# Optimization experiments

Hardware: AMD Instinct MI355X
Metric: run time of the kernel (lower is better)

The kernel has to match this reference:

```python
import jax, jax.numpy as jnp
import numpy as np

EMBED_DIM = 8
THRESHOLD = 0.8
N_NODES = 8192
# QCNNModel (stack of FC layers mimicking quantum conv/pool steps):
# 8 -> 16 -> 16 -> 12 -> 8 -> 4 -> 1, tanh hidden activations, sigmoid head.
QCNN_DIMS = [8, 16, 16, 12, 8, 4, 1]


def setup_inputs() -> dict:
    key = jax.random.key(0)
    ks = jax.random.split(key, 20)
    inp = {
        "inputs": jax.random.normal(ks[0], (N_NODES, EMBED_DIM), dtype=jnp.float32),
        "rotation": jax.random.normal(ks[1], (EMBED_DIM, EMBED_DIM), dtype=jnp.float32),
        "entangle": jax.random.normal(ks[2], (EMBED_DIM, EMBED_DIM), dtype=jnp.float32),
        "gnn_w": jax.random.normal(ks[3], (EMBED_DIM, EMBED_DIM), dtype=jnp.float32) * 0.3,
        "gnn_b": jnp.zeros((EMBED_DIM,), dtype=jnp.float32),
    }
    for li in range(len(QCNN_DIMS) - 1):
        din, dout = QCNN_DIMS[li], QCNN_DIMS[li + 1]
        inp[f"qw{li}"] = jax.random.normal(ks[4 + 2 * li], (dout, din), dtype=jnp.float32) * (1.0 / np.sqrt(din))
        inp[f"qb{li}"] = jnp.zeros((dout,), dtype=jnp.float32)
    return inp


def _forward(inputs, rotation, entangle, gnn_w, gnn_b, qws, qbs):
    n = inputs.shape[0]
    # --- fidelity adjacency (vectorized Gram matrix + threshold) ---
    x = inputs / (jnp.linalg.norm(inputs, axis=1, keepdims=True) + 1e-12)
    fid = jnp.square(x @ x.T)                      # [n, n] |<i|j>|^2
    eye = jnp.eye(n, dtype=bool)
    adj = jnp.where((fid >= THRESHOLD) & ~eye, 1.0, 0.0).astype(inputs.dtype)
    # --- graph diffusion: neighbour sum + linear + relu ---
    neighbour_sum = adj @ inputs                   # [n, d]
    diffused = jax.nn.relu(neighbour_sum @ gnn_w.T + gnn_b)
    # --- self-attention (query=rotation, key=entangle, value=features) ---
    q = diffused @ rotation                        # [n, d]
    k = diffused @ entangle                        # [n, d]
    scores = jax.nn.softmax((q @ k.T) / jnp.sqrt(jnp.asarray(EMBED_DIM, inputs.dtype)), axis=-1)
    attended = scores @ diffused                   # [n, d]
    # --- QCNN fully-connected stack ---
    h = attended
    n_layers = len(qws)
    for li in range(n_layers):
        h = h @ qws[li].T + qbs[li]
        h = jax.nn.tanh(h) if li < n_layers - 1 else jax.nn.sigmoid(h)
    return h                                       # [n, 1]


def reference(inputs, rotation, entangle, gnn_w, gnn_b,
              qw0, qb0, qw1, qb1, qw2, qb2, qw3, qb3, qw4, qb4, qw5, qb5):
    qws = [qw0, qw1, qw2, qw3, qw4, qw5]
    qbs = [qb0, qb1, qb2, qb3, qb4, qb5]
    return _forward(inputs, rotation, entangle, gnn_w, gnn_b, qws, qbs)
```

## Files before the change

### kernel.cpp

```cpp
#include <hip/hip_runtime.h>
#include <math.h>

#define NN 8192

__device__ __forceinline__ float fexp2(float x) {
    float r;
    asm("v_exp_f32 %0, %1" : "=v"(r) : "v"(x));
    return r;
}

__global__ __launch_bounds__(256) void k_norm(const float* __restrict__ in,
                                              float* __restrict__ xn) {
    int r = blockIdx.x * 256 + threadIdx.x;
    const float4* p = reinterpret_cast<const float4*>(in + (size_t)r * 8);
    float4 a = p[0], b = p[1];
    float ss = a.x*a.x + a.y*a.y + a.z*a.z + a.w*a.w
             + b.x*b.x + b.y*b.y + b.z*b.z + b.w*b.w;
    float inv = 1.0f / (sqrtf(ss) + 1e-12f);
    a.x *= inv; a.y *= inv; a.z *= inv; a.w *= inv;
    b.x *= inv; b.y *= inv; b.z *= inv; b.w *= inv;
    float4* o = reinterpret_cast<float4*>(xn + (size_t)r * 8);
    o[0] = a; o[1] = b;
}

template<int SEGS>
__global__ __launch_bounds__(256) void k_adj_t(const float* __restrict__ xn,
                                               const float* __restrict__ in,
                                               float* __restrict__ pns) {
    constexpr int JC = NN / SEGS;
    constexpr int RSTR = NN / 2;
    __shared__ float4 sx[JC * 2];
    __shared__ float4 si[JC * 2];
    int tid = threadIdx.x;
    int r = blockIdx.x * 256 + tid;
    int seg = blockIdx.y;
    int j0 = seg * JC;

    for (int idx = tid; idx < JC * 2; idx += 256) {
        sx[idx] = reinterpret_cast<const float4*>(xn + (size_t)j0 * 8)[idx];
        si[idx] = reinterpret_cast<const float4*>(in + (size_t)j0 * 8)[idx];
    }
    float x[2][8];
    #pragma unroll
    for (int i = 0; i < 2; ++i) {
        const float4* xp = reinterpret_cast<const float4*>(xn + (size_t)(r + i * RSTR) * 8);
        float4 a = xp[0], b = xp[1];
        x[i][0]=a.x; x[i][1]=a.y; x[i][2]=a.z; x[i][3]=a.w;
        x[i][4]=b.x; x[i][5]=b.y; x[i][6]=b.z; x[i][7]=b.w;
    }
    __syncthreads();

    float A[2][8] = {};

    for (int c8 = 0; c8 < JC; c8 += 8) {
        #pragma unroll
        for (int u = 0; u < 8; ++u) {
            int t = c8 + u;
            int j = j0 + t;
            float4 a = sx[t * 2], b = sx[t * 2 + 1];
            bool hit[2];
            bool hany = false;
            #pragma unroll
            for (int i = 0; i < 2; ++i) {
                float d = fmaf(x[i][7], b.w, fmaf(x[i][6], b.z,
                          fmaf(x[i][5], b.y, fmaf(x[i][4], b.x,
                          fmaf(x[i][3], a.w, fmaf(x[i][2], a.z,
                          fmaf(x[i][1], a.y, x[i][0] * a.x)))))));
                hit[i] = (d * d >= 0.8f) && (j != r + i * RSTR);
                hany = hany || hit[i];
            }
            if (hany) {
                float4 u0 = si[t * 2], u1 = si[t * 2 + 1];
                #pragma unroll
                for (int i = 0; i < 2; ++i) {
                    if (hit[i]) {
                        A[i][0]+=u0.x; A[i][1]+=u0.y; A[i][2]+=u0.z; A[i][3]+=u0.w;
                        A[i][4]+=u1.x; A[i][5]+=u1.y; A[i][6]+=u1.z; A[i][7]+=u1.w;
                    }
                }
            }
        }
    }
    #pragma unroll
    for (int i = 0; i < 2; ++i) {
        float4* o = reinterpret_cast<float4*>(pns + ((size_t)(r + i * RSTR) * SEGS + seg) * 8);
        o[0] = make_float4(A[i][0], A[i][1], A[i][2], A[i][3]);
        o[1] = make_float4(A[i][4], A[i][5], A[i][6], A[i][7]);
    }
}

template<int NSEG>
__global__ __launch_bounds__(256) void k_diff3(const float* __restrict__ pns,
                                               const float* __restrict__ gw,
                                               const float* __restrict__ gb,
                                               const float* __restrict__ rot,
                                               const float* __restrict__ ent,
                                               float* __restrict__ dif,
                                               float* __restrict__ qsb,
                                               float* __restrict__ kkb) {
    int tid = threadIdx.x;
    int sub = tid & 31;
    int row = blockIdx.x * 8 + (tid >> 5);
    float ns[8] = {0,0,0,0,0,0,0,0};
    #pragma unroll
    for (int it = 0; it < NSEG / 32; ++it) {
        int g = sub + it * 32;
        const float4* p = reinterpret_cast<const float4*>(pns + ((size_t)row * NSEG + g) * 8);
        float4 a = p[0], b = p[1];
        ns[0]+=a.x; ns[1]+=a.y; ns[2]+=a.z; ns[3]+=a.w;
        ns[4]+=b.x; ns[5]+=b.y; ns[6]+=b.z; ns[7]+=b.w;
    }
    #pragma unroll
    for (int msk = 1; msk <= 16; msk <<= 1) {
        #pragma unroll
        for (int e = 0; e < 8; ++e) ns[e] += __shfl_xor(ns[e], msk);
    }
    if (sub == 0) {
        float df[8];
        #pragma unroll
        for (int d = 0; d < 8; ++d) {
            float v = gb[d];
            #pragma unroll
            for (int e = 0; e < 8; ++e) v += ns[e] * gw[d * 8 + e];
            df[d] = fmaxf(v, 0.0f);
        }
        const float QSC = (float)(1.4426950408889634 / 2.8284271247461903);
        #pragma unroll
        for (int d = 0; d < 8; ++d) {
            float vq = 0.0f, vk = 0.0f;
            #pragma unroll
            for (int e = 0; e < 8; ++e) {
                vq += df[e] * rot[e * 8 + d];
                vk += df[e] * ent[e * 8 + d];
            }
            qsb[(size_t)row * 8 + d] = vq * QSC;
            kkb[(size_t)row * 8 + d] = vk;
        }
        float4* o = reinterpret_cast<float4*>(dif + (size_t)row * 8);
        o[0] = make_float4(df[0], df[1], df[2], df[3]);
        o[1] = make_float4(df[4], df[5], df[6], df[7]);
    }
}

template<int SEGS>
__global__ __launch_bounds__(256) void k_attn_t(const float* __restrict__ qsb,
                                                const float* __restrict__ kkb,
                                                const float* __restrict__ dif,
                                                float* __restrict__ pacc,
                                                float* __restrict__ pm,
                                                float* __restrict__ psum) {
    constexpr int JC = NN / SEGS;
    constexpr int RSTR = NN / 2;
    __shared__ float4 sk[JC * 2];
    __shared__ float4 sd[JC * 2];
    int tid = threadIdx.x;
    int r = blockIdx.x * 256 + tid;
    int seg = blockIdx.y;
    int j0 = seg * JC;

    for (int idx = tid; idx < JC * 2; idx += 256) {
        sk[idx] = reinterpret_cast<const float4*>(kkb + (size_t)j0 * 8)[idx];
        sd[idx] = reinterpret_cast<const float4*>(dif + (size_t)j0 * 8)[idx];
    }
    float q[2][8];
    #pragma unroll
    for (int i = 0; i < 2; ++i) {
        const float4* qp = reinterpret_cast<const float4*>(qsb + (size_t)(r + i * RSTR) * 8);
        float4 a = qp[0], b = qp[1];
        q[i][0]=a.x; q[i][1]=a.y; q[i][2]=a.z; q[i][3]=a.w;
        q[i][4]=b.x; q[i][5]=b.y; q[i][6]=b.z; q[i][7]=b.w;
    }
    __syncthreads();

    float m[2], sum[2];
    float A[2][8] = {};
    #pragma unroll
    for (int i = 0; i < 2; ++i) { m[i] = -__builtin_huge_valf(); sum[i] = 0.0f; }

    for (int c8 = 0; c8 < JC; c8 += 8) {
        float s[2][8];
        #pragma unroll
        for (int u = 0; u < 8; ++u) {
            int t = c8 + u;
            float4 ka = sk[t * 2], kb = sk[t * 2 + 1];
            #pragma unroll
            for (int i = 0; i < 2; ++i) {
                s[i][u] = fmaf(q[i][7], kb.w, fmaf(q[i][6], kb.z,
                          fmaf(q[i][5], kb.y, fmaf(q[i][4], kb.x,
                          fmaf(q[i][3], ka.w, fmaf(q[i][2], ka.z,
                          fmaf(q[i][1], ka.y, q[i][0] * ka.x)))))));
            }
        }
        #pragma unroll
        for (int i = 0; i < 2; ++i) {
            float cm = fmaxf(fmaxf(fmaxf(s[i][0], s[i][1]), fmaxf(s[i][2], s[i][3])),
                             fmaxf(fmaxf(s[i][4], s[i][5]), fmaxf(s[i][6], s[i][7])));
            float mn = fmaxf(m[i], cm);
            float rs = fexp2(m[i] - mn);
            m[i] = mn;
            sum[i] *= rs;
            #pragma unroll
            for (int e = 0; e < 8; ++e) A[i][e] *= rs;
        }
        #pragma unroll
        for (int u = 0; u < 8; ++u) {
            int t = c8 + u;
            float4 da = sd[t * 2], db = sd[t * 2 + 1];
            #pragma unroll
            for (int i = 0; i < 2; ++i) {
                float p = fexp2(s[i][u] - m[i]);
                sum[i] += p;
                A[i][0] = fmaf(p, da.x, A[i][0]); A[i][1] = fmaf(p, da.y, A[i][1]);
                A[i][2] = fmaf(p, da.z, A[i][2]); A[i][3] = fmaf(p, da.w, A[i][3]);
                A[i][4] = fmaf(p, db.x, A[i][4]); A[i][5] = fmaf(p, db.y, A[i][5]);
                A[i][6] = fmaf(p, db.z, A[i][6]); A[i][7] = fmaf(p, db.w, A[i][7]);
            }
        }
    }

    #pragma unroll
    for (int i = 0; i < 2; ++i) {
        size_t b = (size_t)(r + i * RSTR) * SEGS + seg;
        float4* o = reinterpret_cast<float4*>(pacc + b * 8);
        o[0] = make_float4(A[i][0], A[i][1], A[i][2], A[i][3]);
        o[1] = make_float4(A[i][4], A[i][5], A[i][6], A[i][7]);
        pm[b] = m[i];
        psum[b] = sum[i];
    }
}

template<int NSEG>
__global__ __launch_bounds__(256) void k_merge3(const float* __restrict__ pacc,
                                                const float* __restrict__ pm,
                                                const float* __restrict__ psum,
                                                const float* __restrict__ qw0, const float* __restrict__ qb0,
                                                const float* __restrict__ qw1, const float* __restrict__ qb1,
                                                const float* __restrict__ qw2, const float* __restrict__ qb2,
                                                const float* __restrict__ qw3, const float* __restrict__ qb3,
                                                const float* __restrict__ qw4, const float* __restrict__ qb4,
                                                const float* __restrict__ qw5, const float* __restrict__ qb5,
                                                float* __restrict__ out) {
    int tid = threadIdx.x;
    int sub = tid & 31;
    int row = blockIdx.x * 8 + (tid >> 5);

    float m = -3.0e38f, T = 0.0f;
    float A[8] = {0,0,0,0,0,0,0,0};
    #pragma unroll
    for (int it = 0; it < NSEG / 32; ++it) {
        int g = sub + it * 32;
        size_t base = (size_t)row * NSEG + g;
        float mg = pm[base];
        float newm = fmaxf(m, mg);
        float cs = fexp2(m - newm);
        float cg = fexp2(mg - newm);
        T = fmaf(T, cs, psum[base] * cg);
        const float4* p = reinterpret_cast<const float4*>(pacc + base * 8);
        float4 a = p[0], b = p[1];
        A[0] = fmaf(A[0], cs, a.x * cg); A[1] = fmaf(A[1], cs, a.y * cg);
        A[2] = fmaf(A[2], cs, a.z * cg); A[3] = fmaf(A[3], cs, a.w * cg);
        A[4] = fmaf(A[4], cs, b.x * cg); A[5] = fmaf(A[5], cs, b.y * cg);
        A[6] = fmaf(A[6], cs, b.z * cg); A[7] = fmaf(A[7], cs, b.w * cg);
        m = newm;
    }
    #pragma unroll
    for (int msk = 1; msk <= 16; msk <<= 1) {
        float mo = __shfl_xor(m, msk);
        float To = __shfl_xor(T, msk);
        float Ao[8];
        #pragma unroll
        for (int e = 0; e < 8; ++e) Ao[e] = __shfl_xor(A[e], msk);
        float newm = fmaxf(m, mo);
        float cs = fexp2(m - newm);
        float co = fexp2(mo - newm);
        T = T * cs + To * co;
        #pragma unroll
        for (int e = 0; e < 8; ++e) A[e] = A[e] * cs + Ao[e] * co;
        m = newm;
    }

    if (sub == 0) {
        float invT = 1.0f / T;
        float h0[8];
        #pragma unroll
        for (int d = 0; d < 8; ++d) h0[d] = A[d] * invT;

        float h1[16];
        #pragma unroll
        for (int t = 0; t < 16; ++t) {
            float v = qb0[t];
            #pragma unroll
            for (int e = 0; e < 8; ++e) v += h0[e] * qw0[t * 8 + e];
            h1[t] = tanhf(v);
        }
        float h2[16];
        #pragma unroll
        for (int t = 0; t < 16; ++t) {
            float v = qb1[t];
            #pragma unroll
            for (int e = 0; e < 16; ++e) v += h1[e] * qw1[t * 16 + e];
            h2[t] = tanhf(v);
        }
        float h3[12];
        #pragma unroll
        for (int t = 0; t < 12; ++t) {
            float v = qb2[t];
            #pragma unroll
            for (int e = 0; e < 16; ++e) v += h2[e] * qw2[t * 16 + e];
            h3[t] = tanhf(v);
        }
        float h4[8];
        #pragma unroll
        for (int t = 0; t < 8; ++t) {
            float v = qb3[t];
            #pragma unroll
            for (int e = 0; e < 12; ++e) v += h3[e] * qw3[t * 12 + e];
            h4[t] = tanhf(v);
        }
        float h5[4];
        #pragma unroll
        for (int t = 0; t < 4; ++t) {
            float v = qb4[t];
            #pragma unroll
            for (int e = 0; e < 8; ++e) v += h4[e] * qw4[t * 8 + e];
            h5[t] = tanhf(v);
        }
        float o = qb5[0];
        #pragma unroll
        for (int e = 0; e < 4; ++e) o += h5[e] * qw5[e];
        out[row] = 1.0f / (1.0f + expf(-o));
    }
}

extern "C" void kernel_launch(void* const* d_in, const int* in_sizes, int n_in,
                              void* d_out, int out_size, void* d_ws, size_t ws_size,
                              hipStream_t stream) {
    const float* in  = (const float*)d_in[0];
    const float* rot = (const float*)d_in[1];
    const float* ent = (const float*)d_in[2];
    const float* gw  = (const float*)d_in[3];
    const float* gb  = (const float*)d_in[4];
    const float* qw0 = (const float*)d_in[5];
    const float* qb0 = (const float*)d_in[6];
    const float* qw1 = (const float*)d_in[7];
    const float* qb1 = (const float*)d_in[8];
    const float* qw2 = (const float*)d_in[9];
    const float* qb2 = (const float*)d_in[10];
    const float* qw3 = (const float*)d_in[11];
    const float* qb3 = (const float*)d_in[12];
    const float* qw4 = (const float*)d_in[13];
    const float* qb4 = (const float*)d_in[14];
    const float* qw5 = (const float*)d_in[15];
    const float* qb5 = (const float*)d_in[16];

    auto need = [](int nseg) { return ((size_t)NN * 8 * 4 + (size_t)nseg * NN * 18) * 4; };
    const int nseg = (ws_size >= need(64)) ? 64 : 32;

    float* ws = (float*)d_ws;
    size_t off = 0;
    float* xn   = ws + off; off += (size_t)NN * 8;
    float* pns  = ws + off; off += (size_t)nseg * NN * 8;
    float* dif  = ws + off; off += (size_t)NN * 8;
    float* qsb  = ws + off; off += (size_t)NN * 8;
    float* kkb  = ws + off; off += (size_t)NN * 8;
    float* pacc = ws + off; off += (size_t)nseg * NN * 8;
    float* pm   = ws + off; off += (size_t)nseg * NN;
    float* psum = ws + off; off += (size_t)nseg * NN;

    dim3 blk(256);
    k_norm<<<dim3(NN / 256), blk, 0, stream>>>(in, xn);
    if (nseg == 64) {
        k_adj_t<64><<<dim3(NN / 2 / 256, 64), blk, 0, stream>>>(xn, in, pns);
        k_diff3<64><<<dim3(NN / 8), blk, 0, stream>>>(pns, gw, gb, rot, ent, dif, qsb, kkb);
        k_attn_t<64><<<dim3(NN / 2 / 256, 64), blk, 0, stream>>>(qsb, kkb, dif, pacc, pm, psum);
        k_merge3<64><<<dim3(NN / 8), blk, 0, stream>>>(pacc, pm, psum,
                                                       qw0, qb0, qw1, qb1, qw2, qb2,
                                                       qw3, qb3, qw4, qb4, qw5, qb5,
                                                       (float*)d_out);
    } else {
        k_adj_t<32><<<dim3(NN / 2 / 256, 32), blk, 0, stream>>>(xn, in, pns);
        k_diff3<32><<<dim3(NN / 8), blk, 0, stream>>>(pns, gw, gb, rot, ent, dif, qsb, kkb);
        k_attn_t<32><<<dim3(NN / 2 / 256, 32), blk, 0, stream>>>(qsb, kkb, dif, pacc, pm, psum);
        k_merge3<32><<<dim3(NN / 8), blk, 0, stream>>>(pacc, pm, psum,
                                                       qw0, qb0, qw1, qb1, qw2, qb2,
                                                       qw3, qb3, qw4, qb4, qw5, qb5,
                                                       (float*)d_out);
    }
}
```

Baseline: 100.8 us.

## Run attention QK^T and PV on fp16 MFMA with padded transposed operands

Replaces the scalar fp32 flash-style attention kernel with one that computes scores and the probability-value product via 16x16x16 fp16 MFMA instructions, one wave per 16 query rows. The diffusion kernel now emits fp16 Q/K padded to 16 dims and a transposed fp16 value matrix in place of the fp32 buffers. The aim is to move the O(N^2) dot-product and accumulation work onto matrix cores and cut the LDS traffic. In exchange it reads K and V straight from global memory without LDS staging, doubles the padded work, and lowers the precision of scores and probabilities to fp16.

```diff
diff --git a/kernel.cpp b/kernel.cpp
--- a/kernel.cpp
+++ b/kernel.cpp
@@ -2,6 +2,9 @@
 #include <math.h>
 
 #define NN 8192
+
+typedef _Float16 h4v __attribute__((ext_vector_type(4)));
+typedef float f4v __attribute__((ext_vector_type(4)));
 
 __device__ __forceinline__ float fexp2(float x) {
     float r;
@@ -95,9 +98,9 @@
                                                const float* __restrict__ gb,
                                                const float* __restrict__ rot,
                                                const float* __restrict__ ent,
-                                               float* __restrict__ dif,
-                                               float* __restrict__ qsb,
-                                               float* __restrict__ kkb) {
+                                               _Float16* __restrict__ qhp,
+                                               _Float16* __restrict__ khp,
+                                               _Float16* __restrict__ difT) {
     int tid = threadIdx.x;
     int sub = tid & 31;
     int row = blockIdx.x * 8 + (tid >> 5);
@@ -133,99 +136,75 @@
                 vq += df[e] * rot[e * 8 + d];
                 vk += df[e] * ent[e * 8 + d];
             }
-            qsb[(size_t)row * 8 + d] = vq * QSC;
-            kkb[(size_t)row * 8 + d] = vk;
-        }
-        float4* o = reinterpret_cast<float4*>(dif + (size_t)row * 8);
-        o[0] = make_float4(df[0], df[1], df[2], df[3]);
-        o[1] = make_float4(df[4], df[5], df[6], df[7]);
+            qhp[(size_t)row * 16 + d] = (_Float16)(vq * QSC);
+            khp[(size_t)row * 16 + d] = (_Float16)vk;
+            difT[(size_t)d * NN + row] = (_Float16)df[d];
+        }
+        #pragma unroll
+        for (int d = 8; d < 16; ++d) {
+            qhp[(size_t)row * 16 + d] = (_Float16)0.0f;
+            khp[(size_t)row * 16 + d] = (_Float16)0.0f;
+            difT[(size_t)d * NN + row] = (_Float16)0.0f;
+        }
     }
 }
 
 template<int SEGS>
-__global__ __launch_bounds__(256) void k_attn_t(const float* __restrict__ qsb,
-                                                const float* __restrict__ kkb,
-                                                const float* __restrict__ dif,
+__global__ __launch_bounds__(256) void k_attn_m(const _Float16* __restrict__ qhp,
+                                                const _Float16* __restrict__ khp,
+                                                const _Float16* __restrict__ difT,
                                                 float* __restrict__ pacc,
                                                 float* __restrict__ pm,
                                                 float* __restrict__ psum) {
     constexpr int JC = NN / SEGS;
-    constexpr int RSTR = NN / 2;
-    __shared__ float4 sk[JC * 2];
-    __shared__ float4 sd[JC * 2];
     int tid = threadIdx.x;
-    int r = blockIdx.x * 256 + tid;
+    int lane = tid & 63;
+    int w = tid >> 6;
+    int qbase = (blockIdx.x * 4 + w) * 16;
     int seg = blockIdx.y;
     int j0 = seg * JC;
-
-    for (int idx = tid; idx < JC * 2; idx += 256) {
-        sk[idx] = reinterpret_cast<const float4*>(kkb + (size_t)j0 * 8)[idx];
-        sd[idx] = reinterpret_cast<const float4*>(dif + (size_t)j0 * 8)[idx];
-    }
-    float q[2][8];
-    #pragma unroll
-    for (int i = 0; i < 2; ++i) {
-        const float4* qp = reinterpret_cast<const float4*>(qsb + (size_t)(r + i * RSTR) * 8);
-        float4 a = qp[0], b = qp[1];
-        q[i][0]=a.x; q[i][1]=a.y; q[i][2]=a.z; q[i][3]=a.w;
-        q[i][4]=b.x; q[i][5]=b.y; q[i][6]=b.z; q[i][7]=b.w;
-    }
-    __syncthreads();
-
-    float m[2], sum[2];
-    float A[2][8] = {};
-    #pragma unroll
-    for (int i = 0; i < 2; ++i) { m[i] = -__builtin_huge_valf(); sum[i] = 0.0f; }
-
-    for (int c8 = 0; c8 < JC; c8 += 8) {
-        float s[2][8];
-        #pragma unroll
-        for (int u = 0; u < 8; ++u) {
-            int t = c8 + u;
-            float4 ka = sk[t * 2], kb = sk[t * 2 + 1];
-            #pragma unroll
-            for (int i = 0; i < 2; ++i) {
-                s[i][u] = fmaf(q[i][7], kb.w, fmaf(q[i][6], kb.z,
-                          fmaf(q[i][5], kb.y, fmaf(q[i][4], kb.x,
-                          fmaf(q[i][3], ka.w, fmaf(q[i][2], ka.z,
-                          fmaf(q[i][1], ka.y, q[i][0] * ka.x)))))));
-            }
-        }
-        #pragma unroll
-        for (int i = 0; i < 2; ++i) {
-            float cm = fmaxf(fmaxf(fmaxf(s[i][0], s[i][1]), fmaxf(s[i][2], s[i][3])),
-                             fmaxf(fmaxf(s[i][4], s[i][5]), fmaxf(s[i][6], s[i][7])));
-            float mn = fmaxf(m[i], cm);
-            float rs = fexp2(m[i] - mn);
-            m[i] = mn;
-            sum[i] *= rs;
-            #pragma unroll
-            for (int e = 0; e < 8; ++e) A[i][e] *= rs;
-        }
-        #pragma unroll
-        for (int u = 0; u < 8; ++u) {
-            int t = c8 + u;
-            float4 da = sd[t * 2], db = sd[t * 2 + 1];
-            #pragma unroll
-            for (int i = 0; i < 2; ++i) {
-                float p = fexp2(s[i][u] - m[i]);
-                sum[i] += p;
-                A[i][0] = fmaf(p, da.x, A[i][0]); A[i][1] = fmaf(p, da.y, A[i][1]);
-                A[i][2] = fmaf(p, da.z, A[i][2]); A[i][3] = fmaf(p, da.w, A[i][3]);
-                A[i][4] = fmaf(p, db.x, A[i][4]); A[i][5] = fmaf(p, db.y, A[i][5]);
-                A[i][6] = fmaf(p, db.z, A[i][6]); A[i][7] = fmaf(p, db.w, A[i][7]);
-            }
-        }
-    }
-
-    #pragma unroll
-    for (int i = 0; i < 2; ++i) {
-        size_t b = (size_t)(r + i * RSTR) * SEGS + seg;
-        float4* o = reinterpret_cast<float4*>(pacc + b * 8);
-        o[0] = make_float4(A[i][0], A[i][1], A[i][2], A[i][3]);
-        o[1] = make_float4(A[i][4], A[i][5], A[i][6], A[i][7]);
-        pm[b] = m[i];
-        psum[b] = sum[i];
+    int l15 = lane & 15;
+    int kgrp = lane >> 4;
+
+    h4v qv = *reinterpret_cast<const h4v*>(qhp + (size_t)(qbase + l15) * 16 + kgrp * 4);
+
+    float m = -3.0e38f, sum = 0.0f;
+    f4v O = {0.0f, 0.0f, 0.0f, 0.0f};
+
+    for (int t = 0; t < JC / 16; ++t) {
+        int kb = j0 + t * 16;
+        h4v kv = *reinterpret_cast<const h4v*>(khp + (size_t)(kb + l15) * 16 + kgrp * 4);
+        f4v s = __builtin_amdgcn_mfma_f32_16x16x16f16(kv, qv, (f4v){0.f,0.f,0.f,0.f}, 0, 0, 0);
+
+        float tm = fmaxf(fmaxf(s[0], s[1]), fmaxf(s[2], s[3]));
+        tm = fmaxf(tm, __shfl_xor(tm, 16));
+        tm = fmaxf(tm, __shfl_xor(tm, 32));
+        float mn = fmaxf(m, tm);
+        float rs = fexp2(m - mn);
+        m = mn;
+        float p0 = fexp2(s[0] - mn);
+        float p1 = fexp2(s[1] - mn);
+        float p2 = fexp2(s[2] - mn);
+        float p3 = fexp2(s[3] - mn);
+        sum = fmaf(sum, rs, (p0 + p1) + (p2 + p3));
+        h4v pa = {(_Float16)p0, (_Float16)p1, (_Float16)p2, (_Float16)p3};
+
+        h4v dv = *reinterpret_cast<const h4v*>(difT + (size_t)l15 * NN + kb + kgrp * 4);
+        O[0] *= rs; O[1] *= rs; O[2] *= rs; O[3] *= rs;
+        O = __builtin_amdgcn_mfma_f32_16x16x16f16(dv, pa, O, 0, 0, 0);
+    }
+
+    sum += __shfl_xor(sum, 16);
+    sum += __shfl_xor(sum, 32);
+
+    size_t b = (size_t)(qbase + l15) * SEGS + seg;
+    if (lane < 32) {
+        float4* o = reinterpret_cast<float4*>(pacc + b * 8 + kgrp * 4);
+        *o = make_float4(O[0], O[1], O[2], O[3]);
+    }
+    if (lane < 16) {
+        pm[b] = m;
+        psum[b] = sum;
     }
 }
 
@@ -293,20 +272,20 @@
             for (int e = 0; e < 8; ++e) v += h0[e] * qw0[t * 8 + e];
             h1[t] = tanhf(v);
         }
-        float h2[16];
+        float h2x[16];
         #pragma unroll
         for (int t = 0; t < 16; ++t) {
             float v = qb1[t];
             #pragma unroll
             for (int e = 0; e < 16; ++e) v += h1[e] * qw1[t * 16 + e];
-            h2[t] = tanhf(v);
+            h2x[t] = tanhf(v);
         }
         float h3[12];
         #pragma unroll
         for (int t = 0; t < 12; ++t) {
             float v = qb2[t];
             #pragma unroll
-            for (int e = 0; e < 16; ++e) v += h2[e] * qw2[t * 16 + e];
+            for (int e = 0; e < 16; ++e) v += h2x[e] * qw2[t * 16 + e];
             h3[t] = tanhf(v);
         }
         float h4[8];
@@ -360,9 +339,9 @@
     size_t off = 0;
     float* xn   = ws + off; off += (size_t)NN * 8;
     float* pns  = ws + off; off += (size_t)nseg * NN * 8;
-    float* dif  = ws + off; off += (size_t)NN * 8;
-    float* qsb  = ws + off; off += (size_t)NN * 8;
-    float* kkb  = ws + off; off += (size_t)NN * 8;
+    _Float16* qhp  = (_Float16*)(ws + off); off += (size_t)NN * 8;
+    _Float16* khp  = (_Float16*)(ws + off); off += (size_t)NN * 8;
+    _Float16* difT = (_Float16*)(ws + off); off += (size_t)NN * 8;
     float* pacc = ws + off; off += (size_t)nseg * NN * 8;
     float* pm   = ws + off; off += (size_t)nseg * NN;
     float* psum = ws + off; off += (size_t)nseg * NN;
@@ -371,16 +350,16 @@
     k_norm<<<dim3(NN / 256), blk, 0, stream>>>(in, xn);
     if (nseg == 64) {
         k_adj_t<64><<<dim3(NN / 2 / 256, 64), blk, 0, stream>>>(xn, in, pns);
-        k_diff3<64><<<dim3(NN / 8), blk, 0, stream>>>(pns, gw, gb, rot, ent, dif, qsb, kkb);
-        k_attn_t<64><<<dim3(NN / 2 / 256, 64), blk, 0, stream>>>(qsb, kkb, dif, pacc, pm, psum);
+        k_diff3<64><<<dim3(NN / 8), blk, 0, stream>>>(pns, gw, gb, rot, ent, qhp, khp, difT);
+        k_attn_m<64><<<dim3(NN / 64, 64), blk, 0, stream>>>(qhp, khp, difT, pacc, pm, psum);
         k_merge3<64><<<dim3(NN / 8), blk, 0, stream>>>(pacc, pm, psum,
                                                        qw0, qb0, qw1, qb1, qw2, qb2,
                                                        qw3, qb3, qw4, qb4, qw5, qb5,
                                                        (float*)d_out);
     } else {
         k_adj_t<32><<<dim3(NN / 2 / 256, 32), blk, 0, stream>>>(xn, in, pns);
-        k_diff3<32><<<dim3(NN / 8), blk, 0, stream>>>(pns, gw, gb, rot, ent, dif, qsb, kkb);
-        k_attn_t<32><<<dim3(NN / 2 / 256, 32), blk, 0, stream>>>(qsb, kkb, dif, pacc, pm, psum);
+        k_diff3<32><<<dim3(NN / 8), blk, 0, stream>>>(pns, gw, gb, rot, ent, qhp, khp, difT);
+        k_attn_m<32><<<dim3(NN / 64, 32), blk, 0, stream>>>(qhp, khp, difT, pacc, pm, psum);
         k_merge3<32><<<dim3(NN / 8), blk, 0, stream>>>(pacc, pm, psum,
                                                        qw0, qb0, qw1, qb1, qw2, qb2,
                                                        qw3, qb3, qw4, qb4, qw5, qb5,
```

After: 108.5 us. 7.6% more time.
